# Kernel tuning notes

Hardware: AMD Instinct MI355X
Metric: run time of the kernel (lower is better)

Reference implementation:

```python
import jax, jax.numpy as jnp
import numpy as np
from jax import lax

DIM = 128
K = 3
PAD = K // 2


def setup_inputs() -> dict:
    key = jax.random.key(0)
    k1, k2, k3, k4, k5 = jax.random.split(key, 5)
    B, H, W = 64, 32, 32
    wdim = DIM * DIM * K * K + DIM  # 147584
    # scale question_rep (it encodes conv weights) for numerical sanity
    question_rep = jax.random.normal(k1, (B, wdim), dtype=jnp.float32) * 0.05
    lhs_rep = jax.random.normal(k2, (B, DIM, H, W), dtype=jnp.float32)
    rhs_rep = jax.random.normal(k3, (B, DIM, H, W), dtype=jnp.float32)
    proj_w = jax.random.normal(k4, (DIM, 2 * DIM), dtype=jnp.float32) * (1.0 / np.sqrt(2 * DIM))
    proj_b = jax.random.normal(k5, (DIM,), dtype=jnp.float32) * 0.01
    return {"question_rep": question_rep, "lhs_rep": lhs_rep,
            "rhs_rep": rhs_rep, "proj_w": proj_w, "proj_b": proj_b}


def _per_sample_conv(x, w, b):
    # x: [dim, H, W], w: [dim, dim, K, K], b: [dim]
    y = lax.conv_general_dilated(
        x[None], w, window_strides=(1, 1),
        padding=[(PAD, PAD), (PAD, PAD)],
        dimension_numbers=("NCHW", "OIHW", "NCHW"))
    return y[0] + b[:, None, None]


def reference(question_rep, lhs_rep, rhs_rep, proj_w, proj_b):
    B = question_rep.shape[0]
    wdim = DIM * DIM * K * K
    cnn_weight = question_rep[:, :wdim].reshape(B, DIM, DIM, K, K)
    cnn_bias = question_rep[:, wdim:]  # [B, dim]
    # 1x1 projection conv: cat along channels then contract
    cat = jnp.concatenate([lhs_rep, rhs_rep], axis=1)  # [B, 2*dim, H, W]
    cnn_inp = jnp.einsum("bchw,oc->bohw", cat, proj_w) + proj_b[None, :, None, None]
    # per-sample dynamic conv, vectorized over batch (equiv. grouped conv)
    out = jax.vmap(_per_sample_conv)(cnn_inp, cnn_weight, cnn_bias)
    return out
```

## Files before the change

### kernel.cpp

```cpp
#include <hip/hip_runtime.h>
#include <hip/hip_bf16.h>

#define QSTRIDE 147584
#define WOFF    147456

typedef __attribute__((ext_vector_type(8))) short bf16x8;
typedef __attribute__((ext_vector_type(4))) float f32x4;

static __device__ __forceinline__ ushort f2bf(float f) {
  union { float f; unsigned u; } x; x.f = f;
  unsigned r = x.u + 0x7fffu + ((x.u >> 16) & 1u);
  return (ushort)(r >> 16);
}
static __device__ __forceinline__ unsigned pk2(ushort a, ushort b) {
  return (unsigned)a | ((unsigned)b << 16);
}

__global__ __launch_bounds__(256) void pack_w_kernel(const float* __restrict__ q,
                                                     ushort* __restrict__ wt2) {
  __shared__ float  Ls[4608];
  __shared__ ushort Lw[9 * 4 * 16 * 32];
  int b = blockIdx.x >> 3, ogrp = blockIdx.x & 7;
  int t = threadIdx.x;
  const float* gbase = q + (size_t)b * QSTRIDE + (size_t)ogrp * 16 * 1152;
  int o_loc = t >> 6;
  int ci    = (t & 63) * 2;
  int cq    = ci >> 5, coff = ci & 31;
  for (int r = 0; r < 4; ++r) {
    __syncthreads();
    const float* gs = gbase + r * 4608;
#pragma unroll
    for (int i = 0; i < 18; ++i) Ls[i * 256 + t] = gs[i * 256 + t];
    __syncthreads();
    int o_in = r * 4 + o_loc;
    const float* v = Ls + o_loc * 1152 + ci * 9;
    float a[18];
#pragma unroll
    for (int i = 0; i < 18; ++i) a[i] = v[i];
#pragma unroll
    for (int tap = 0; tap < 9; ++tap) {
      unsigned pkv = pk2(f2bf(a[tap]), f2bf(a[9 + tap]));
      *(unsigned*)&Lw[((tap * 4 + cq) * 16 + o_in) * 32 + coff] = pkv;
    }
  }
  __syncthreads();
  int wv = t >> 6, l = t & 63;
  ushort* dstb = wt2 + (size_t)b * 147456 + (size_t)ogrp * 16 * 32;
#pragma unroll
  for (int tap = 0; tap < 9; ++tap) {
    const uint4 val = *(const uint4*)&Lw[(tap * 4 + wv) * 512 + l * 8];
    *(uint4*)(dstb + (size_t)(tap * 4 + wv) * 4096 + l * 8) = val;
  }
}

__global__ __launch_bounds__(256) void pack_pw_kernel(const float* __restrict__ pw,
                                                      ushort* __restrict__ pwb2) {
  int tg = blockIdx.x * 256 + threadIdx.x;
  int o  = tg >> 5;
  int c0 = (tg & 31) * 8;
  const float4* s4 = (const float4*)(pw + (size_t)o * 256 + c0);
  float4 f0 = s4[0], f1 = s4[1];
  uint4 pkv;
  pkv.x = pk2(f2bf(f0.x), f2bf(f0.y)); pkv.y = pk2(f2bf(f0.z), f2bf(f0.w));
  pkv.z = pk2(f2bf(f1.x), f2bf(f1.y)); pkv.w = pk2(f2bf(f1.z), f2bf(f1.w));
  *(uint4*)(pwb2 + (size_t)(c0 >> 5) * 4096 + o * 32 + (c0 & 31)) = pkv;
}

__global__ __launch_bounds__(256) void transpose_x_kernel(const float* __restrict__ lhs,
                                                          const float* __restrict__ rhs,
                                                          ushort* __restrict__ xt) {
  __shared__ ushort Ts[32][132];
  int b = blockIdx.y;
  int c = blockIdx.x & 7, half = blockIdx.x >> 3;
  const float* src = (c < 4 ? lhs : rhs) + (size_t)b * 131072 + (size_t)(c & 3) * 32768;
  ushort* dst = xt + (size_t)(b * 8 + c) * 32768;
  int t = threadIdx.x;
  int chw = t >> 3, pxg = (t & 7) * 16;
  int pxr = t >> 1, chr = (t & 1) * 16;
#pragma unroll
  for (int pt = 0; pt < 4; ++pt) {
    int p0 = half * 512 + pt * 128;
    if (pt) __syncthreads();
    const float* s = src + (size_t)chw * 1024 + p0 + pxg;
#pragma unroll
    for (int i = 0; i < 4; ++i) {
      float4 f = *(const float4*)(s + 4 * i);
      uint2 pk;
      pk.x = pk2(f2bf(f.x), f2bf(f.y));
      pk.y = pk2(f2bf(f.z), f2bf(f.w));
      *(uint2*)&Ts[chw][pxg + 4 * i] = pk;
    }
    __syncthreads();
    ushort g[16];
#pragma unroll
    for (int j = 0; j < 16; ++j) g[j] = Ts[chr + j][pxr];
    *(uint4*)(dst + (size_t)(p0 + pxr) * 32 + chr)     = *(uint4*)&g[0];
    *(uint4*)(dst + (size_t)(p0 + pxr) * 32 + chr + 8) = *(uint4*)&g[8];
  }
}

__global__ __launch_bounds__(256, 2) void fused_conv_kernel(const ushort* __restrict__ wt2,
                                                            const ushort* __restrict__ pwb2,
                                                            const ushort* __restrict__ xt,
                                                            const float* __restrict__ pb,
                                                            const float* __restrict__ q,
                                                            float* __restrict__ out) {
  __shared__ ushort Bs[4][6][34][32];
  int blk = blockIdx.x;
  int b = blk & 63, tile = blk >> 6;
  int p0 = tile * 128, h0 = tile * 4;
  int t = threadIdx.x;
  int lane = t & 63, wv = t >> 6;
  int quad = lane >> 4, li = lane & 15;

  if (t < 48) {
    int cq = t & 3, side = (t >> 2) & 1, rr = t >> 3;
    uint4* z4 = (uint4*)&Bs[cq][rr][side ? 33 : 0][0];
    uint4 z; z.x = z.y = z.z = z.w = 0u;
    z4[0] = z; z4[1] = z; z4[2] = z; z4[3] = z;
  }

  {
    int rk[3], wk[3], hk[3]; bool lv[3];
#pragma unroll
    for (int k = 0; k < 3; ++k) {
      int nt = wv * 3 + k;
      rk[k] = nt >> 1;
      wk[k] = (nt & 1) * 16;
      hk[k] = h0 - 1 + rk[k];
      lv[k] = (hk[k] >= 0) && (hk[k] < 32);
    }
    const ushort* xtb = xt + (size_t)b * 8 * 32768;
    f32x4 acc[3][8] = {};
#pragma unroll
    for (int c = 0; c < 8; ++c) {
      bf16x8 bg[3];
#pragma unroll
      for (int k = 0; k < 3; ++k) {
        union { uint4 u; bf16x8 v; } bu;
        if (lv[k]) {
          int px = hk[k] * 32 + wk[k] + li;
          bu.u = *(const uint4*)(xtb + ((size_t)c * 1024 + px) * 32 + quad * 8);
        } else {
          bu.u.x = bu.u.y = bu.u.z = bu.u.w = 0u;
        }
        bg[k] = bu.v;
      }
      const ushort* ap = pwb2 + (size_t)c * 4096 + li * 32 + quad * 8;
#pragma unroll
      for (int mi = 0; mi < 8; ++mi) {
        bf16x8 af = *(const bf16x8*)(ap + mi * 512);
#pragma unroll
        for (int k = 0; k < 3; ++k)
          acc[k][mi] = __builtin_amdgcn_mfma_f32_16x16x32_bf16(af, bg[k], acc[k][mi], 0, 0, 0);
      }
    }
#pragma unroll
    for (int k = 0; k < 3; ++k) {
#pragma unroll
      for (int mi = 0; mi < 8; ++mi) {
        int o0 = mi * 16 + quad * 4;
        uint2 pkv;
        if (lv[k]) {
          float4 bias = *(const float4*)(pb + o0);
          f32x4 a = acc[k][mi];
          pkv.x = pk2(f2bf(a.x + bias.x), f2bf(a.y + bias.y));
          pkv.y = pk2(f2bf(a.z + bias.z), f2bf(a.w + bias.w));
        } else {
          pkv.x = 0u; pkv.y = 0u;
        }
        *(uint2*)&Bs[o0 >> 5][rk[k]][wk[k] + li + 1][o0 & 31] = pkv;
      }
    }
  }
  __syncthreads();

  int m0 = (wv & 1) * 64, n0 = (wv >> 1) * 64;
  f32x4 acc2[4][4] = {};
  const ushort* wtb = wt2 + (size_t)b * 147456;
#pragma unroll
  for (int cq = 0; cq < 4; ++cq) {
    const ushort* wcq = wtb + (size_t)cq * 4096;
#pragma unroll
    for (int tap = 0; tap < 9; ++tap) {
      const ushort* ar = wcq + (size_t)tap * 16384;
      int kh = tap / 3, kw = tap - kh * 3;
      bf16x8 af[4], bg[4];
#pragma unroll
      for (int mi = 0; mi < 4; ++mi)
        af[mi] = *(const bf16x8*)(ar + (m0 + mi*16 + li) * 32 + quad * 8);
#pragma unroll
      for (int ni = 0; ni < 4; ++ni) {
        int pl = n0 + ni*16 + li;
        int hh = pl >> 5, ww = pl & 31;
        bg[ni] = *(const bf16x8*)&Bs[cq][hh + kh][ww + kw][quad * 8];
      }
#pragma unroll
      for (int mi = 0; mi < 4; ++mi)
#pragma unroll
        for (int ni = 0; ni < 4; ++ni)
          acc2[mi][ni] = __builtin_amdgcn_mfma_f32_16x16x32_bf16(af[mi], bg[ni], acc2[mi][ni], 0, 0, 0);
    }
  }

  const float* qb = q + (size_t)b * QSTRIDE + WOFF;
  float* ob = out + (size_t)b * 128 * 1024 + p0;
#pragma unroll
  for (int mi = 0; mi < 4; ++mi) {
    int o0 = m0 + mi*16 + quad*4;
    float4 bias = *(const float4*)(qb + o0);
#pragma unroll
    for (int ni = 0; ni < 4; ++ni) {
      int pl = n0 + ni*16 + li;
      float* dp = ob + (size_t)o0 * 1024 + pl;
      f32x4 a = acc2[mi][ni];
      dp[0]    = a.x + bias.x;
      dp[1024] = a.y + bias.y;
      dp[2048] = a.z + bias.z;
      dp[3072] = a.w + bias.w;
    }
  }
}

extern "C" void kernel_launch(void* const* d_in, const int* in_sizes, int n_in,
                              void* d_out, int out_size, void* d_ws, size_t ws_size,
                              hipStream_t stream) {
  const float* q   = (const float*)d_in[0];
  const float* lhs = (const float*)d_in[1];
  const float* rhs = (const float*)d_in[2];
  const float* pw  = (const float*)d_in[3];
  const float* pb  = (const float*)d_in[4];
  float* out = (float*)d_out;

  char* ws = (char*)d_ws;
  ushort* wt2  = (ushort*)(ws);
  ushort* pwb2 = (ushort*)(ws + 18874368);
  ushort* xt   = (ushort*)(ws + 18939904);

  pack_w_kernel     <<<512, 256, 0, stream>>>(q, wt2);
  pack_pw_kernel    <<<16,  256, 0, stream>>>(pw, pwb2);
  transpose_x_kernel<<<dim3(16, 64), 256, 0, stream>>>(lhs, rhs, xt);
  fused_conv_kernel <<<512, 256, 0, stream>>>(wt2, pwb2, xt, pb, q, out);
}
```

Before: 186.8 us.

## Stage conv weights and input tiles into LDS via async global-to-LDS pipeline

The fused conv kernel now prefetches the projection input rows into shared memory with global_load_lds before the 1x1 projection. It then streams the per-sample 3x3 weight slices through a 5-slot LDS ring buffer, issuing loads four steps ahead, with hand-placed vmcnt waits and barriers. This is meant to hide global-memory latency for the weight operand that was previously loaded directly from global in the inner MFMA loop. In exchange, LDS use grows to about 136KB and occupancy drops to one block per CU, and the hand-written waitcnt sequence has to stay exactly matched to the load count.

Result: slower. 207.1 us (+10.9%).

```diff
diff --git a/kernel.cpp b/kernel.cpp
--- a/kernel.cpp
+++ b/kernel.cpp
@@ -15,6 +15,13 @@
 static __device__ __forceinline__ unsigned pk2(ushort a, ushort b) {
   return (unsigned)a | ((unsigned)b << 16);
 }
+static __device__ __forceinline__ void async16(const ushort* g, ushort* l) {
+  __builtin_amdgcn_global_load_lds((const __attribute__((address_space(1))) void*)g,
+                                   (__attribute__((address_space(3))) void*)l, 16, 0, 0);
+}
+#define WAITBAR_(vm) asm volatile("s_waitcnt vmcnt(" #vm ") lgkmcnt(0)\n\ts_barrier" ::: "memory")
+#define WAITBAR(vm) WAITBAR_(vm)
+#define BARSYNC() asm volatile("s_waitcnt lgkmcnt(0)\n\ts_barrier" ::: "memory")
 
 __global__ __launch_bounds__(256) void pack_w_kernel(const float* __restrict__ q,
                                                      ushort* __restrict__ wt2) {
@@ -99,109 +106,150 @@
   }
 }
 
-__global__ __launch_bounds__(256, 2) void fused_conv_kernel(const ushort* __restrict__ wt2,
+__global__ __launch_bounds__(256, 1) void fused_conv_kernel(const ushort* __restrict__ wt2,
                                                             const ushort* __restrict__ pwb2,
                                                             const ushort* __restrict__ xt,
                                                             const float* __restrict__ pb,
                                                             const float* __restrict__ q,
                                                             float* __restrict__ out) {
-  __shared__ ushort Bs[4][6][34][32];
+  __shared__ ushort LDSP[69632];
+  ushort* Xs = LDSP;
+  ushort* Bs = LDSP;
+  ushort* Ar = LDSP + 49152;
+#define BSOFF(cq, r, p, ch) ((((cq) * 6 + (r)) * 34 + (p)) * 32 + (ch))
   int blk = blockIdx.x;
   int b = blk & 63, tile = blk >> 6;
   int p0 = tile * 128, h0 = tile * 4;
   int t = threadIdx.x;
   int lane = t & 63, wv = t >> 6;
   int quad = lane >> 4, li = lane & 15;
+  const ushort* wtb = wtb = wt2 + (size_t)b * 147456;
+  const ushort* xtb = xt + (size_t)b * 8 * 32768;
+
+#pragma unroll
+  for (int cc = 0; cc < 2; ++cc) {
+    int c = wv + cc * 4;
+    const ushort* xs = xtb + (size_t)c * 32768;
+    ushort* xd = Xs + c * 6144;
+#pragma unroll
+    for (int i = 0; i < 12; ++i) {
+      int r = i >> 1;
+      int h = h0 - 1 + r; h = h < 0 ? 0 : (h > 31 ? 31 : h);
+      int pxg = h * 32 + (i & 1) * 16;
+      async16(xs + (size_t)pxg * 32 + lane * 8, xd + i * 512);
+    }
+  }
+#pragma unroll
+  for (int s = 0; s < 4; ++s) {
+    const ushort* ag = wtb + (size_t)((s % 9) * 4 + (s / 9)) * 4096;
+    ushort* ad = Ar + (s % 5) * 4096 + wv * 1024;
+    async16(ag + (size_t)(wv * 2) * 512 + lane * 8,       ad);
+    async16(ag + (size_t)(wv * 2 + 1) * 512 + lane * 8,   ad + 512);
+  }
+  WAITBAR(8);
+
+  int rk[3], wk[3]; bool lv[3];
+#pragma unroll
+  for (int k = 0; k < 3; ++k) {
+    int nt = wv * 3 + k;
+    rk[k] = nt >> 1;
+    wk[k] = (nt & 1) * 16;
+    int hk = h0 - 1 + rk[k];
+    lv[k] = (hk >= 0) && (hk < 32);
+  }
+  f32x4 acc[3][8] = {};
+#pragma unroll
+  for (int c = 0; c < 8; ++c) {
+    bf16x8 bg[3];
+#pragma unroll
+    for (int k = 0; k < 3; ++k) {
+      union { uint4 u; bf16x8 v; } bu;
+      if (lv[k]) {
+        int pl = rk[k] * 32 + wk[k] + li;
+        bu.u = *(const uint4*)(Xs + (size_t)c * 6144 + pl * 32 + quad * 8);
+      } else {
+        bu.u.x = bu.u.y = bu.u.z = bu.u.w = 0u;
+      }
+      bg[k] = bu.v;
+    }
+    const ushort* ap = pwb2 + (size_t)c * 4096 + li * 32 + quad * 8;
+#pragma unroll
+    for (int mi = 0; mi < 8; ++mi) {
+      bf16x8 af = *(const bf16x8*)(ap + mi * 512);
+#pragma unroll
+      for (int k = 0; k < 3; ++k)
+        acc[k][mi] = __builtin_amdgcn_mfma_f32_16x16x32_bf16(af, bg[k], acc[k][mi], 0, 0, 0);
+    }
+  }
+
+  BARSYNC();
 
   if (t < 48) {
     int cq = t & 3, side = (t >> 2) & 1, rr = t >> 3;
-    uint4* z4 = (uint4*)&Bs[cq][rr][side ? 33 : 0][0];
+    uint4* z4 = (uint4*)&Bs[BSOFF(cq, rr, side ? 33 : 0, 0)];
     uint4 z; z.x = z.y = z.z = z.w = 0u;
     z4[0] = z; z4[1] = z; z4[2] = z; z4[3] = z;
   }
-
-  {
-    int rk[3], wk[3], hk[3]; bool lv[3];
-#pragma unroll
-    for (int k = 0; k < 3; ++k) {
-      int nt = wv * 3 + k;
-      rk[k] = nt >> 1;
-      wk[k] = (nt & 1) * 16;
-      hk[k] = h0 - 1 + rk[k];
-      lv[k] = (hk[k] >= 0) && (hk[k] < 32);
-    }
-    const ushort* xtb = xt + (size_t)b * 8 * 32768;
-    f32x4 acc[3][8] = {};
-#pragma unroll
-    for (int c = 0; c < 8; ++c) {
-      bf16x8 bg[3];
-#pragma unroll
-      for (int k = 0; k < 3; ++k) {
-        union { uint4 u; bf16x8 v; } bu;
-        if (lv[k]) {
-          int px = hk[k] * 32 + wk[k] + li;
-          bu.u = *(const uint4*)(xtb + ((size_t)c * 1024 + px) * 32 + quad * 8);
-        } else {
-          bu.u.x = bu.u.y = bu.u.z = bu.u.w = 0u;
-        }
-        bg[k] = bu.v;
+#pragma unroll
+  for (int k = 0; k < 3; ++k) {
+#pragma unroll
+    for (int mi = 0; mi < 8; ++mi) {
+      int o0 = mi * 16 + quad * 4;
+      uint2 pkv;
+      if (lv[k]) {
+        float4 bias = *(const float4*)(pb + o0);
+        f32x4 a = acc[k][mi];
+        pkv.x = pk2(f2bf(a.x + bias.x), f2bf(a.y + bias.y));
+        pkv.y = pk2(f2bf(a.z + bias.z), f2bf(a.w + bias.w));
+      } else {
+        pkv.x = 0u; pkv.y = 0u;
       }
-      const ushort* ap = pwb2 + (size_t)c * 4096 + li * 32 + quad * 8;
-#pragma unroll
-      for (int mi = 0; mi < 8; ++mi) {
-        bf16x8 af = *(const bf16x8*)(ap + mi * 512);
-#pragma unroll
-        for (int k = 0; k < 3; ++k)
-          acc[k][mi] = __builtin_amdgcn_mfma_f32_16x16x32_bf16(af, bg[k], acc[k][mi], 0, 0, 0);
-      }
-    }
-#pragma unroll
-    for (int k = 0; k < 3; ++k) {
-#pragma unroll
-      for (int mi = 0; mi < 8; ++mi) {
-        int o0 = mi * 16 + quad * 4;
-        uint2 pkv;
-        if (lv[k]) {
-          float4 bias = *(const float4*)(pb + o0);
-          f32x4 a = acc[k][mi];
-          pkv.x = pk2(f2bf(a.x + bias.x), f2bf(a.y + bias.y));
-          pkv.y = pk2(f2bf(a.z + bias.z), f2bf(a.w + bias.w));
-        } else {
-          pkv.x = 0u; pkv.y = 0u;
-        }
-        *(uint2*)&Bs[o0 >> 5][rk[k]][wk[k] + li + 1][o0 & 31] = pkv;
-      }
-    }
-  }
-  __syncthreads();
+      *(uint2*)&Bs[BSOFF(o0 >> 5, rk[k], wk[k] + li + 1, o0 & 31)] = pkv;
+    }
+  }
+  BARSYNC();
 
   int m0 = (wv & 1) * 64, n0 = (wv >> 1) * 64;
   f32x4 acc2[4][4] = {};
-  const ushort* wtb = wt2 + (size_t)b * 147456;
-#pragma unroll
-  for (int cq = 0; cq < 4; ++cq) {
-    const ushort* wcq = wtb + (size_t)cq * 4096;
-#pragma unroll
-    for (int tap = 0; tap < 9; ++tap) {
-      const ushort* ar = wcq + (size_t)tap * 16384;
-      int kh = tap / 3, kw = tap - kh * 3;
-      bf16x8 af[4], bg[4];
-#pragma unroll
-      for (int mi = 0; mi < 4; ++mi)
-        af[mi] = *(const bf16x8*)(ar + (m0 + mi*16 + li) * 32 + quad * 8);
-#pragma unroll
-      for (int ni = 0; ni < 4; ++ni) {
-        int pl = n0 + ni*16 + li;
-        int hh = pl >> 5, ww = pl & 31;
-        bg[ni] = *(const bf16x8*)&Bs[cq][hh + kh][ww + kw][quad * 8];
-      }
-#pragma unroll
-      for (int mi = 0; mi < 4; ++mi)
-#pragma unroll
-        for (int ni = 0; ni < 4; ++ni)
-          acc2[mi][ni] = __builtin_amdgcn_mfma_f32_16x16x32_bf16(af[mi], bg[ni], acc2[mi][ni], 0, 0, 0);
-    }
-  }
+
+#define CSTEP(s, vm) do { \
+    WAITBAR(vm); \
+    if ((s) + 4 <= 35) { \
+      const int sn = (s) + 4; \
+      const ushort* ag = wtb + (size_t)((sn % 9) * 4 + (sn / 9)) * 4096; \
+      ushort* ad = Ar + (sn % 5) * 4096 + wv * 1024; \
+      async16(ag + (size_t)(wv * 2) * 512 + lane * 8,     ad); \
+      async16(ag + (size_t)(wv * 2 + 1) * 512 + lane * 8, ad + 512); \
+    } \
+    __builtin_amdgcn_sched_barrier(0); \
+    { const int cq_ = (s) / 9, tap_ = (s) % 9; \
+      const int kh_ = tap_ / 3, kw_ = tap_ % 3; \
+      const ushort* ar = Ar + ((s) % 5) * 4096; \
+      bf16x8 af[4], bg[4]; \
+      _Pragma("unroll") \
+      for (int mi = 0; mi < 4; ++mi) \
+        af[mi] = *(const bf16x8*)(ar + (m0 + mi*16 + li) * 32 + quad * 8); \
+      _Pragma("unroll") \
+      for (int ni = 0; ni < 4; ++ni) { \
+        int pl = n0 + ni*16 + li; \
+        int hh = pl >> 5, ww = pl & 31; \
+        bg[ni] = *(const bf16x8*)&Bs[BSOFF(cq_, hh + kh_, ww + kw_, quad * 8)]; \
+      } \
+      _Pragma("unroll") \
+      for (int mi = 0; mi < 4; ++mi) \
+        _Pragma("unroll") \
+        for (int ni = 0; ni < 4; ++ni) \
+          acc2[mi][ni] = __builtin_amdgcn_mfma_f32_16x16x32_bf16(af[mi], bg[ni], acc2[mi][ni], 0, 0, 0); \
+    } \
+  } while (0)
+
+  CSTEP( 0,6); CSTEP( 1,6); CSTEP( 2,6); CSTEP( 3,6); CSTEP( 4,6); CSTEP( 5,6);
+  CSTEP( 6,6); CSTEP( 7,6); CSTEP( 8,6); CSTEP( 9,6); CSTEP(10,6); CSTEP(11,6);
+  CSTEP(12,6); CSTEP(13,6); CSTEP(14,6); CSTEP(15,6); CSTEP(16,6); CSTEP(17,6);
+  CSTEP(18,6); CSTEP(19,6); CSTEP(20,6); CSTEP(21,6); CSTEP(22,6); CSTEP(23,6);
+  CSTEP(24,6); CSTEP(25,6); CSTEP(26,6); CSTEP(27,6); CSTEP(28,6); CSTEP(29,6);
+  CSTEP(30,6); CSTEP(31,6); CSTEP(32,6); CSTEP(33,4); CSTEP(34,2); CSTEP(35,0);
+#undef CSTEP
 
   const float* qb = q + (size_t)b * QSTRIDE + WOFF;
   float* ob = out + (size_t)b * 128 * 1024 + p0;
@@ -220,6 +268,7 @@
       dp[3072] = a.w + bias.w;
     }
   }
+#undef BSOFF
 }
 
 extern "C" void kernel_launch(void* const* d_in, const int* in_sizes, int n_in,
```
